# Kernel tuning notes

Measured on AMD Instinct MI355X. Metric: run time of the kernel, lower is better.

## Reference

```python
import jax, jax.numpy as jnp
import numpy as np
import math

N_NODES = 50000
N_EDGES = 800000
N_GRAPHS = 2500
IN_DIM = 128
HID = 128
HEADS = 2


def _lin_params(key, fan_in, fan_out, bias=True):
    k1, k2 = jax.random.split(key)
    s = 1.0 / math.sqrt(fan_in)
    W = jax.random.uniform(k1, (fan_in, fan_out), jnp.float32, -s, s)
    b = jax.random.uniform(k2, (fan_out,), jnp.float32, -s, s) if bias else None
    return W, b


def setup_inputs() -> dict:
    key = jax.random.key(0)
    ks = jax.random.split(key, 16)
    x = jax.random.normal(ks[0], (N_NODES, IN_DIM), jnp.float32)
    edge_index = jax.random.randint(ks[1], (2, N_EDGES), 0, N_NODES, jnp.int64)
    batch = jnp.sort(jax.random.randint(ks[2], (N_NODES,), 0, N_GRAPHS, jnp.int64))
    edge_attr = jax.random.normal(ks[3], (N_EDGES,), jnp.float32)

    HC = HEADS * HID  # 256
    # layer 1: in=128, out_channels=128, heads=2, concat=True
    Wq1, bq1 = _lin_params(ks[4], IN_DIM, HC)
    Wk1, bk1 = _lin_params(ks[5], IN_DIM, HC)
    Wv1, bv1 = _lin_params(ks[6], IN_DIM, HC)
    We1, _ = _lin_params(ks[7], 1, HC, bias=False)
    Ws1, bs1 = _lin_params(ks[8], IN_DIM, HC)
    # layer 2: in=256, out_channels=128, heads=2, concat=False
    Wq2, bq2 = _lin_params(ks[9], HC, HC)
    Wk2, bk2 = _lin_params(ks[10], HC, HC)
    Wv2, bv2 = _lin_params(ks[11], HC, HC)
    We2, _ = _lin_params(ks[12], 1, HC, bias=False)
    Ws2, bs2 = _lin_params(ks[13], HC, HID)
    return {
        "x": x, "edge_index": edge_index, "batch": batch, "edge_attr": edge_attr,
        "Wq1": Wq1, "bq1": bq1, "Wk1": Wk1, "bk1": bk1, "Wv1": Wv1, "bv1": bv1,
        "We1": We1, "Ws1": Ws1, "bs1": bs1,
        "Wq2": Wq2, "bq2": bq2, "Wk2": Wk2, "bk2": bk2, "Wv2": Wv2, "bv2": bv2,
        "We2": We2, "Ws2": Ws2, "bs2": bs2,
    }


def transformer_conv(x, src, dst, edge_attr, Wq, bq, Wk, bk, Wv, bv, We, Ws, bs,
                     heads, out_ch, concat):
    N = x.shape[0]
    q = (x @ Wq + bq).reshape(N, heads, out_ch)
    k = (x @ Wk + bk).reshape(N, heads, out_ch)
    v = (x @ Wv + bv).reshape(N, heads, out_ch)
    e = (edge_attr @ We).reshape(-1, heads, out_ch)  # [E,H,C]
    kj = k[src] + e
    vj = v[src] + e
    alpha = jnp.einsum('ehc,ehc->eh', q[dst], kj) / math.sqrt(out_ch)  # [E,H]
    amax = jax.ops.segment_max(alpha, dst, num_segments=N)  # [N,H]
    ex = jnp.exp(alpha - amax[dst])
    denom = jax.ops.segment_sum(ex, dst, num_segments=N)  # [N,H]
    w = ex / denom[dst]  # segment softmax over incoming edges
    out = jax.ops.segment_sum(w[..., None] * vj, dst, num_segments=N)  # [N,H,C]
    out = out.reshape(N, heads * out_ch) if concat else out.mean(axis=1)
    return out + (x @ Ws + bs)  # root/skip connection (beta=False)


def reference(x, edge_index, batch, edge_attr,
              Wq1, bq1, Wk1, bk1, Wv1, bv1, We1, Ws1, bs1,
              Wq2, bq2, Wk2, bk2, Wv2, bv2, We2, Ws2, bs2):
    src, dst = edge_index[0], edge_index[1]
    ea = edge_attr.reshape(-1, 1)
    h = transformer_conv(x, src, dst, ea, Wq1, bq1, Wk1, bk1, Wv1, bv1, We1,
                         Ws1, bs1, HEADS, HID, concat=True)
    h = jax.nn.relu(h)  # dropout = identity in eval mode
    h = transformer_conv(h, src, dst, ea, Wq2, bq2, Wk2, bk2, Wv2, bv2, We2,
                         Ws2, bs2, HEADS, HID, concat=False)
    # global mean pool per graph
    sums = jax.ops.segment_sum(h, batch, num_segments=N_GRAPHS)
    cnts = jax.ops.segment_sum(jnp.ones((h.shape[0],), h.dtype), batch,
                               num_segments=N_GRAPHS)
    return sums / jnp.maximum(cnts, 1.0)[:, None]
```

## Files before the change

kernel.cpp:

```cpp
#include <hip/hip_runtime.h>
#include <math.h>

#define N_NODES  50000
#define N_EDGES  800000
#define N_GRAPHS 2500
#define IN_DIM   128
#define HID      128
#define HEADS    2
#define HC       256

typedef unsigned short u16;
typedef unsigned char  u8;
typedef unsigned int   u32;
typedef short  s8v  __attribute__((ext_vector_type(8)));
typedef float  f4v  __attribute__((ext_vector_type(4)));
typedef float  f2v  __attribute__((ext_vector_type(2)));

__device__ inline float bf2f(u16 u) {
    union { unsigned int i; float f; } c; c.i = ((unsigned int)u) << 16; return c.f;
}
__device__ inline u16 f2bf(float x) {
    union { float f; unsigned int i; } c; c.f = x;
    unsigned int r = c.i + 0x7FFFu + ((c.i >> 16) & 1u);
    return (u16)(r >> 16);
}
__device__ inline float bflo(unsigned int u) {
    union { unsigned int i; float f; } c; c.i = u << 16; return c.f;
}
__device__ inline float bfhi(unsigned int u) {
    union { unsigned int i; float f; } c; c.i = u & 0xffff0000u; return c.f;
}
__device__ inline f2v mkf2(float a, float b) { f2v r; r.x = a; r.y = b; return r; }

#if __has_builtin(__builtin_amdgcn_cvt_pk_fp8_f32) && __has_builtin(__builtin_amdgcn_cvt_pk_f32_fp8)
#define FP8_HW 1
#else
#define FP8_HW 0
#endif

__device__ inline u8 f2fp8(float x) {
#if FP8_HW
    return (u8)(__builtin_amdgcn_cvt_pk_fp8_f32(x, x, 0, false) & 0xff);
#else
    union { float f; unsigned int u; } c; c.f = x;
    unsigned int s = (c.u >> 24) & 0x80u;
    c.u &= 0x7fffffffu;
    if (c.f >= 448.f) return (u8)(s | 0x7e);
    if (c.f < 0.015625f) {
        int m = (int)(c.f * 512.f + 0.5f);
        if (m >= 8) return (u8)(s | 0x08);
        return (u8)(s | m);
    }
    c.u += 0x000fffffu + ((c.u >> 20) & 1u);
    unsigned int e = ((c.u >> 23) & 0xffu) - 120u;
    unsigned int m = (c.u >> 20) & 7u;
    return (u8)(s | (e << 3) | m);
#endif
}

__device__ inline void fp8x8_to_f32(uint2 kd8, float* kf) {
#if FP8_HW
    f2v p0 = __builtin_amdgcn_cvt_pk_f32_fp8(kd8.x, false);
    f2v p1 = __builtin_amdgcn_cvt_pk_f32_fp8(kd8.x, true);
    f2v p2 = __builtin_amdgcn_cvt_pk_f32_fp8(kd8.y, false);
    f2v p3 = __builtin_amdgcn_cvt_pk_f32_fp8(kd8.y, true);
    kf[0] = p0.x; kf[1] = p0.y; kf[2] = p1.x; kf[3] = p1.y;
    kf[4] = p2.x; kf[5] = p2.y; kf[6] = p3.x; kf[7] = p3.y;
#else
#pragma unroll
    for (int i = 0; i < 8; ++i) {
        unsigned int b = ((i < 4) ? (kd8.x >> (8 * i)) : (kd8.y >> (8 * (i - 4)))) & 0xffu;
        unsigned int em = b & 0x7fu;
        union { unsigned int u; float f; } c;
        c.u = ((b & 0x80u) << 24) | ((em + 960u) << 20);
        float fn = c.f;
        float fs = (float)(int)em * 0.001953125f;
        fs = (b & 0x80u) ? -fs : fs;
        kf[i] = (em >= 8u) ? fn : fs;
    }
#endif
}

__device__ inline void fp8x8_to_f2(uint2 kd8, f2v* k2) {
#if FP8_HW
    k2[0] = __builtin_amdgcn_cvt_pk_f32_fp8(kd8.x, false);
    k2[1] = __builtin_amdgcn_cvt_pk_f32_fp8(kd8.x, true);
    k2[2] = __builtin_amdgcn_cvt_pk_f32_fp8(kd8.y, false);
    k2[3] = __builtin_amdgcn_cvt_pk_f32_fp8(kd8.y, true);
#else
    float kf[8];
    fp8x8_to_f32(kd8, kf);
    k2[0] = mkf2(kf[0], kf[1]); k2[1] = mkf2(kf[2], kf[3]);
    k2[2] = mkf2(kf[4], kf[5]); k2[3] = mkf2(kf[6], kf[7]);
#endif
}

__global__ __launch_bounds__(256) void init_kernel(
    const int* __restrict__ ei, const int* __restrict__ batch,
    int* __restrict__ deg, int* __restrict__ gdeg,
    int* __restrict__ flag_ei, int* __restrict__ flag_b)
{
    int b = blockIdx.x, t = threadIdx.x;
    if (b < 49) {
        int base = b * 1024 + t * 4;
        if (base + 3 < N_NODES) {
            *(int4*)&deg[base] = make_int4(0, 0, 0, 0);
        } else {
#pragma unroll
            for (int i = 0; i < 4; ++i) if (base + i < N_NODES) deg[base + i] = 0;
        }
    } else if (b < 59) {
        int i = (b - 49) * 256 + t;
        if (i < N_GRAPHS) gdeg[i] = 0;
    } else {
        const int* p = (b == 59) ? ei : batch;
        int ob = (b == 59) ? 1 : 40001;
        int* fl = (b == 59) ? flag_ei : flag_b;
        __shared__ int nz;
        if (t == 0) nz = 0;
        __syncthreads();
        int any = 0;
        for (int i = t; i < 1024; i += 256) if (p[ob + 2 * i] != 0) any = 1;
        if (any) atomicAdd(&nz, 1);
        __syncthreads();
        if (t == 0) *fl = (nz == 0) ? 1 : 0;
    }
}

#define W1_ELEMS (1024 * 128)
#define W2_ELEMS (896 * 256)
__global__ __launch_bounds__(256) void hist_prep_kernel(
    const int* __restrict__ ei, const int* __restrict__ batch,
    const int* __restrict__ flag_ei, const int* __restrict__ flag_b,
    int* __restrict__ deg, int* __restrict__ gdeg,
    const float* __restrict__ Wq1, const float* __restrict__ Wk1,
    const float* __restrict__ Wv1, const float* __restrict__ Ws1,
    const float* __restrict__ bq1, const float* __restrict__ bk1,
    const float* __restrict__ bv1, const float* __restrict__ bs1,
    const float* __restrict__ Wq2, const float* __restrict__ Wk2,
    const float* __restrict__ Wv2, const float* __restrict__ Ws2,
    const float* __restrict__ bq2, const float* __restrict__ bk2,
    const float* __restrict__ bv2, const float* __restrict__ bs2,
    u16* __restrict__ w1T, float* __restrict__ b1cat,
    u16* __restrict__ w2T, float* __restrict__ b2cat)
{
    const int E = N_EDGES;
    int i = blockIdx.x * 256 + threadIdx.x;
    if (i < E) {
        int f = *flag_ei;
        int d = f ? ei[2 * ((size_t)E + i)] : ei[(size_t)E + i];
        if ((unsigned)d < (unsigned)N_NODES) atomicAdd(&deg[d], 1);
    } else if (i < E + N_NODES) {
        int j = i - E;
        int f = *flag_b;
        int g = f ? batch[2 * (size_t)j] : batch[j];
        if ((unsigned)g < (unsigned)N_GRAPHS) atomicAdd(&gdeg[g], 1);
    } else if (i < E + N_NODES + W1_ELEMS) {
        int t1 = i - E - N_NODES;
        int n = t1 >> 7, k = t1 & 127;
        int w = n >> 8, nc = n & 255;
        const float* W = (w == 0) ? Wq1 : (w == 1) ? Wk1 : (w == 2) ? Wv1 : Ws1;
        w1T[t1] = f2bf(W[k * 256 + nc]);
        if (k == 0) {
            const float* b = (w == 0) ? bq1 : (w == 1) ? bk1 : (w == 2) ? bv1 : bs1;
            b1cat[n] = b[nc];
        }
    } else if (i < E + N_NODES + W1_ELEMS + W2_ELEMS) {
        int t2 = i - E - N_NODES - W1_ELEMS;
        int n = t2 >> 8, k = t2 & 255;
        float val, bval;
        if (n < 768) {
            int w = n >> 8, nc = n & 255;
            const float* W = (w == 0) ? Wq2 : (w == 1) ? Wk2 : Wv2;
            val = W[k * 256 + nc];
            bval = ((w == 0) ? bq2 : (w == 1) ? bk2 : bv2)[nc];
        } else {
            val = Ws2[k * 128 + (n - 768)];
            bval = bs2[n - 768];
        }
        w2T[t2] = f2bf(val);
        if (k == 0) b2cat[n] = bval;
    }
}

__global__ void scan_local_kernel(const int* __restrict__ deg, int* __restrict__ rowptr,
                                  int* __restrict__ bsums, int n) {
    __shared__ int sh[256];
    int t = threadIdx.x;
    int base = blockIdx.x * 1024 + t * 4;
    int d0 = (base + 0 < n) ? deg[base + 0] : 0;
    int d1 = (base + 1 < n) ? deg[base + 1] : 0;
    int d2 = (base + 2 < n) ? deg[base + 2] : 0;
    int d3 = (base + 3 < n) ? deg[base + 3] : 0;
    sh[t] = d0 + d1 + d2 + d3;
    __syncthreads();
    for (int off = 1; off < 256; off <<= 1) {
        int val = 0;
        if (t >= off) val = sh[t - off];
        __syncthreads();
        if (t >= off) sh[t] += val;
        __syncthreads();
    }
    int excl = (t > 0) ? sh[t - 1] : 0;
    if (t == 255) bsums[blockIdx.x] = sh[255];
    if (base + 0 < n) rowptr[base + 0] = excl;
    if (base + 1 < n) rowptr[base + 1] = excl + d0;
    if (base + 2 < n) rowptr[base + 2] = excl + d0 + d1;
    if (base + 3 < n) rowptr[base + 3] = excl + d0 + d1 + d2;
}

__global__ __launch_bounds__(256) void scan_mid_kernel(
    int* __restrict__ bsums, int nb, int* __restrict__ rowptr_last,
    const int* __restrict__ gdeg, int* __restrict__ growptr)
{
    int t = threadIdx.x;
    if (blockIdx.x == 0) {
        if (t >= 64) return;
        int v = (t < nb) ? bsums[t] : 0;
        int incl = v;
        for (int off = 1; off < 64; off <<= 1) {
            int u = __shfl_up(incl, off);
            if (t >= off) incl += u;
        }
        if (t < nb) bsums[t] = incl - v;
        if (t == 63) *rowptr_last = incl;
    } else {
        __shared__ int sh[256];
        int base = t * 10;
        int loc[10];
        int s = 0;
#pragma unroll
        for (int i = 0; i < 10; ++i) {
            int v = (base + i < N_GRAPHS) ? gdeg[base + i] : 0;
            loc[i] = s; s += v;
        }
        sh[t] = s;
        __syncthreads();
        for (int off = 1; off < 256; off <<= 1) {
            int val = 0;
            if (t >= off) val = sh[t - off];
            __syncthreads();
            if (t >= off) sh[t] += val;
            __syncthreads();
        }
        int excl = (t > 0) ? sh[t - 1] : 0;
#pragma unroll
        for (int i = 0; i < 10; ++i)
            if (base + i < N_GRAPHS) growptr[base + i] = excl + loc[i];
        if (t == 255) growptr[N_GRAPHS] = sh[255];
    }
}

__global__ void scan_add_kernel(int* __restrict__ rowptr, const int* __restrict__ bsums,
                                int* __restrict__ cursor, int n) {
    int i = blockIdx.x * blockDim.x + threadIdx.x;
    if (i < n) {
        int r = rowptr[i] + bsums[i >> 10];
        rowptr[i] = r;
        cursor[i] = r;
    }
}

template <typename AT, int KDIM, int NT>
__device__ __forceinline__ void gemm_slab_body(
    int bx, const AT* __restrict__ A, const u16* __restrict__ BT,
    const float* __restrict__ biascat,
    u16* __restrict__ C0, u8* __restrict__ KV, u16* __restrict__ C3,
    int s0, int s3, int M)
{
    __shared__ u16 As[64 * KDIM];
    __shared__ u16 Bs[128 * 32];
    int t = threadIdx.x;
    int wid = t >> 6, lane = t & 63;
    int wm = wid >> 1, wn = wid & 1;
    int row0 = bx * 64;

    if constexpr (sizeof(AT) == 4) {
#pragma unroll
        for (int i = 0; i < KDIM / 16; ++i) {
            int c = t + i * 256;
            int row = c / (KDIM / 4);
            int kq  = (c % (KDIM / 4)) * 4;
            float4 d = make_float4(0.f, 0.f, 0.f, 0.f);
            if (row0 + row < M)
                d = *(const float4*)&A[(size_t)(row0 + row) * KDIM + kq];
            ushort4 h;
            h.x = f2bf(d.x); h.y = f2bf(d.y); h.z = f2bf(d.z); h.w = f2bf(d.w);
            *(ushort4*)&As[row * KDIM + (kq ^ ((row & 7) << 3))] = h;
        }
    } else {
#pragma unroll
        for (int i = 0; i < KDIM / 32; ++i) {
            int c = t + i * 256;
            int row = c / (KDIM / 8);
            int kq  = (c % (KDIM / 8)) * 8;
            uint4 d = make_uint4(0u, 0u, 0u, 0u);
            if (row0 + row < M)
                d = *(const uint4*)&A[(size_t)(row0 + row) * KDIM + kq];
            *(uint4*)&As[row * KDIM + (kq ^ ((row & 7) << 3))] = d;
        }
    }
    __syncthreads();

    int koff = (lane >> 4) * 8;
    int mrow = wm * 32 + (lane & 15);
    int nrow = wn * 64 + (lane & 15);
    int aswz = (lane & 7) << 3;
    int bswz = (((lane & 15) >> 1) & 3) << 3;
    int nloc = (lane >> 4) * 4;

    int c0 = t, c1 = t + 256;
    int brow0 = c0 >> 2, bkq0 = (c0 & 3) * 8;
    int brow1 = c1 >> 2, bkq1 = (c1 & 3) * 8;
    int bsa0 = brow0 * 32 + (bkq0 ^ (((brow0 >> 1) & 3) << 3));
    int bsa1 = brow1 * 32 + (bkq1 ^ (((brow1 >> 1) & 3) << 3));

    uint4 pb0 = *(const uint4*)&BT[(size_t)brow0 * KDIM + bkq0];
    uint4 pb1 = *(const uint4*)&BT[(size_t)brow1 * KDIM + bkq1];

    for (int nt = 0; nt < NT; ++nt) {
        f4v acc[2][4];
#pragma unroll
        for (int i = 0; i < 2; ++i)
#pragma unroll
            for (int j = 0; j < 4; ++j)
#pragma unroll
                for (int r = 0; r < 4; ++r) acc[i][j][r] = 0.f;

        for (int k0 = 0; k0 < KDIM; k0 += 32) {
            *(uint4*)&Bs[bsa0] = pb0;
            *(uint4*)&Bs[bsa1] = pb1;
            __syncthreads();

            int nk = k0 + 32, nnt = nt;
            if (nk >= KDIM) { nk = 0; nnt = nt + 1; }
            if (nnt < NT) {
                pb0 = *(const uint4*)&BT[(size_t)(nnt * 128 + brow0) * KDIM + nk + bkq0];
                pb1 = *(const uint4*)&BT[(size_t)(nnt * 128 + brow1) * KDIM + nk + bkq1];
            }

            s8v af[2], bf[4];
#pragma unroll
            for (int tm = 0; tm < 2; ++tm)
                af[tm] = *(const s8v*)&As[(mrow + tm * 16) * KDIM + ((k0 + koff) ^ aswz)];
#pragma unroll
            for (int tn = 0; tn < 4; ++tn)
                bf[tn] = *(const s8v*)&Bs[(nrow + tn * 16) * 32 + (koff ^ bswz)];
#pragma unroll
            for (int tm = 0; tm < 2; ++tm)
#pragma unroll
                for (int tn = 0; tn < 4; ++tn)
                    acc[tm][tn] = __builtin_amdgcn_mfma_f32_16x16x32_bf16(
                        bf[tn], af[tm], acc[tm][tn], 0, 0, 0);
            __syncthreads();
        }

        int buf = nt >> 1;
        int colb = (nt & 1) * 128;
        float4 b4s[4];
#pragma unroll
        for (int tn = 0; tn < 4; ++tn)
            b4s[tn] = *(const float4*)&biascat[nt * 128 + wn * 64 + tn * 16 + nloc];

#pragma unroll
        for (int tm = 0; tm < 2; ++tm) {
            int row = row0 + wm * 32 + tm * 16 + (lane & 15);
            if (row >= M) continue;
#pragma unroll
            for (int tn = 0; tn < 4; ++tn) {
                int ncol = colb + wn * 64 + tn * 16 + nloc;
                float v0 = acc[tm][tn][0] + b4s[tn].x;
                float v1 = acc[tm][tn][1] + b4s[tn].y;
                float v2 = acc[tm][tn][2] + b4s[tn].z;
                float v3 = acc[tm][tn][3] + b4s[tn].w;
                if (buf == 1 || buf == 2) {
                    int off = (buf == 1) ? 0 : 256;
                    u32 pk = (u32)f2fp8(v0) | ((u32)f2fp8(v1) << 8)
                           | ((u32)f2fp8(v2) << 16) | ((u32)f2fp8(v3) << 24);
                    *(u32*)&KV[(size_t)row * 512 + off + ncol] = pk;
                } else {
                    u16* Cp = (buf == 0) ? C0 : C3;
                    int stride = (buf == 0) ? s0 : s3;
                    ushort4 h;
                    h.x = f2bf(v0); h.y = f2bf(v1); h.z = f2bf(v2); h.w = f2bf(v3);
                    *(ushort4*)&Cp[(size_t)row * stride + ncol] = h;
                }
            }
        }
    }
}

#define GB 782

__global__ __launch_bounds__(256, 4) void gemm1_scatter_kernel(
    const float* __restrict__ A, const u16* __restrict__ BT,
    const float* __restrict__ biascat,
    u16* __restrict__ C0, u8* __restrict__ KV, u16* __restrict__ C3,
    int s0, int s3, int M,
    const int* __restrict__ ei, const float* __restrict__ ea,
    const int* __restrict__ flag, int* __restrict__ cursor,
    u32* __restrict__ edges)
{
    if (blockIdx.x < GB) {
        gemm_slab_body<float, 128, 8>(blockIdx.x, A, BT, biascat,
                                      C0, KV, C3, s0, s3, M);
    } else {
        const int E = N_EDGES;
        int i = (blockIdx.x - GB) * 256 + threadIdx.x;
        if (i >= E) return;
        int f = *flag;
        int s = f ? ei[2 * (size_t)i] : ei[i];
        int d = f ? ei[2 * ((size_t)E + i)] : ei[(size_t)E + i];
        if ((unsigned)d >= (unsigned)N_NODES) return;
        if ((unsigned)s >= (unsigned)N_NODES) s = 0;
        int p = atomicAdd(&cursor[d], 1);
        u32 rec = (u32)(s & 0xffff) | ((u32)f2bf(ea[i]) << 16);
        edges[p] = rec;
    }
}

__global__ __launch_bounds__(256, 4) void gemm2_kernel(
    const u16* __restrict__ A, const u16* __restrict__ BT,
    const float* __restrict__ biascat,
    u16* __restrict__ C0, u8* __restrict__ KV, u16* __restrict__ C3,
    int s0, int s3, int M)
{
    gemm_slab_body<u16, 256, 7>(blockIdx.x, A, BT, biascat,
                                C0, KV, C3, s0, s3, M);
}

template <int LAYER>
__global__ __launch_bounds__(256) void attn_node(
    const u16* __restrict__ q, const u8* __restrict__ kv,
    const float* __restrict__ We, const u16* __restrict__ skip,
    const int* __restrict__ rowptr, const u32* __restrict__ edges,
    void* __restrict__ hout, int N)
{
    int wave = (blockIdx.x * blockDim.x + threadIdx.x) >> 6;
    int lane = threadIdx.x & 63;
    if (wave >= N) return;
    int n = wave;
    int half = lane >> 5;
    int cl   = lane & 31;
    const float scale2 = 0.12751743558136835f;

    uint4 qd = *(const uint4*)&q[(size_t)n * HC + cl * 8];
    f2v q2[4];
    q2[0] = mkf2(bflo(qd.x), bfhi(qd.x));
    q2[1] = mkf2(bflo(qd.y), bfhi(qd.y));
    q2[2] = mkf2(bflo(qd.z), bfhi(qd.z));
    q2[3] = mkf2(bflo(qd.w), bfhi(qd.w));
    float4 wlo = *(const float4*)&We[cl * 8];
    float4 whi = *(const float4*)&We[cl * 8 + 4];
    f2v w2[4];
    w2[0] = mkf2(wlo.x, wlo.y); w2[1] = mkf2(wlo.z, wlo.w);
    w2[2] = mkf2(whi.x, whi.y); w2[3] = mkf2(whi.z, whi.w);

    f2v qw2 = q2[0] * w2[0];
    qw2 += q2[1] * w2[1];
    qw2 += q2[2] * w2[2];
    qw2 += q2[3] * w2[3];
    float qw = qw2.x + qw2.y;
    qw += __shfl_xor(qw, 1);
    qw += __shfl_xor(qw, 2);
    qw += __shfl_xor(qw, 4);
    qw += __shfl_xor(qw, 8);

    int e0 = rowptr[n], e1 = rowptr[n + 1];
    float ll0 = 0.f, ll1 = 0.f;
    float pa0 = 0.f, pa1 = 0.f;
    f2v a0[4], a1[4];
#pragma unroll
    for (int i = 0; i < 4; ++i) { a0[i] = mkf2(0.f, 0.f); a1[i] = mkf2(0.f, 0.f); }

    int steps = (e1 - e0 + 7) >> 3;
    for (int st = 0; st < steps; ++st) {
        int eb = e0 + 8 * st + half;
        u32 rec[4]; bool act[4];
#pragma unroll
        for (int j = 0; j < 4; ++j) {
            int ex = eb + 2 * j;
            act[j] = ex < e1;
            rec[j] = edges[act[j] ? ex : e0];
        }
        uint2 kd[4], vd[4]; float ae[4];
#pragma unroll
        for (int j = 0; j < 4; ++j) {
            const u8* base = kv + (size_t)(rec[j] & 0xffffu) * 512;
            kd[j] = *(const uint2*)(base + cl * 8);
            vd[j] = *(const uint2*)(base + 256 + cl * 8);
            ae[j] = bfhi(rec[j]);
        }
#pragma unroll
        for (int j = 0; j < 4; ++j) {
            f2v k2[4], v2[4];
            fp8x8_to_f2(kd[j], k2);
            fp8x8_to_f2(vd[j], v2);
            f2v d2 = q2[0] * k2[0];
            d2 += q2[1] * k2[1];
            d2 += q2[2] * k2[2];
            d2 += q2[3] * k2[3];
            float d = d2.x + d2.y;
            d += __shfl_xor(d, 1);
            d += __shfl_xor(d, 2);
            d += __shfl_xor(d, 4);
            d += __shfl_xor(d, 8);
            float alpha = act[j] ? fmaf(ae[j], qw, d) * scale2 : -16384.f;
            float p = exp2f(fminf(alpha, 80.f));
            f2v p2 = mkf2(p, p);
            if (j & 1) {
                ll1 += p;
                pa1 = fmaf(p, ae[j], pa1);
                a1[0] += p2 * v2[0];
                a1[1] += p2 * v2[1];
                a1[2] += p2 * v2[2];
                a1[3] += p2 * v2[3];
            } else {
                ll0 += p;
                pa0 = fmaf(p, ae[j], pa0);
                a0[0] += p2 * v2[0];
                a0[1] += p2 * v2[1];
                a0[2] += p2 * v2[2];
                a0[3] += p2 * v2[3];
            }
        }
    }

    float l = ll0 + ll1;
    float pa = pa0 + pa1;
    float acc[8];
#pragma unroll
    for (int i = 0; i < 4; ++i) {
        f2v v = a0[i] + a1[i];
        acc[2 * i] = v.x; acc[2 * i + 1] = v.y;
    }

    l += __shfl_xor(l, 32);
    pa += __shfl_xor(pa, 32);
#pragma unroll
    for (int i = 0; i < 8; ++i) acc[i] += __shfl_xor(acc[i], 32);

    float wf[8];
    wf[0] = w2[0].x; wf[1] = w2[0].y; wf[2] = w2[1].x; wf[3] = w2[1].y;
    wf[4] = w2[2].x; wf[5] = w2[2].y; wf[6] = w2[3].x; wf[7] = w2[3].y;

    float inv = (l > 0.f) ? 1.f / l : 0.f;
    float o[8];
#pragma unroll
    for (int i = 0; i < 8; ++i) o[i] = fmaf(pa, wf[i], acc[i]) * inv;

    if constexpr (LAYER == 1) {
        if (half == 0) {
            uint4 sd = *(const uint4*)&skip[(size_t)n * HC + cl * 8];
            float sf[8];
            sf[0] = bflo(sd.x); sf[1] = bfhi(sd.x);
            sf[2] = bflo(sd.y); sf[3] = bfhi(sd.y);
            sf[4] = bflo(sd.z); sf[5] = bfhi(sd.z);
            sf[6] = bflo(sd.w); sf[7] = bfhi(sd.w);
            ushort4 o4a, o4b;
            o4a.x = f2bf(fmaxf(0.f, o[0] + sf[0]));
            o4a.y = f2bf(fmaxf(0.f, o[1] + sf[1]));
            o4a.z = f2bf(fmaxf(0.f, o[2] + sf[2]));
            o4a.w = f2bf(fmaxf(0.f, o[3] + sf[3]));
            o4b.x = f2bf(fmaxf(0.f, o[4] + sf[4]));
            o4b.y = f2bf(fmaxf(0.f, o[5] + sf[5]));
            o4b.z = f2bf(fmaxf(0.f, o[6] + sf[6]));
            o4b.w = f2bf(fmaxf(0.f, o[7] + sf[7]));
            u16* hp = (u16*)hout + (size_t)n * HC + cl * 8;
            *(ushort4*)hp = o4a;
            *(ushort4*)(hp + 4) = o4b;
        }
    } else {
#pragma unroll
        for (int i = 0; i < 8; ++i) {
            float t2 = __shfl_xor(o[i], 16);
            o[i] = 0.5f * (o[i] + t2);
        }
        if (lane < 16) {
            uint4 sd = *(const uint4*)&skip[(size_t)n * HID + lane * 8];
            float sf[8];
            sf[0] = bflo(sd.x); sf[1] = bfhi(sd.x);
            sf[2] = bflo(sd.y); sf[3] = bfhi(sd.y);
            sf[4] = bflo(sd.z); sf[5] = bfhi(sd.z);
            sf[6] = bflo(sd.w); sf[7] = bfhi(sd.w);
            float* hp = (float*)hout + (size_t)n * HID + lane * 8;
            float4 oa, ob;
            oa.x = o[0] + sf[0]; oa.y = o[1] + sf[1];
            oa.z = o[2] + sf[2]; oa.w = o[3] + sf[3];
            ob.x = o[4] + sf[4]; ob.y = o[5] + sf[5];
            ob.z = o[6] + sf[6]; ob.w = o[7] + sf[7];
            *(float4*)hp = oa;
            *(float4*)(hp + 4) = ob;
        }
    }
}

__global__ __launch_bounds__(256) void pool_kernel(
    const float* __restrict__ h2, const int* __restrict__ growptr,
    float* __restrict__ out) {
    int wave = (blockIdx.x * blockDim.x + threadIdx.x) >> 6;
    int lane = threadIdx.x & 63;
    if (wave >= N_GRAPHS) return;
    int r0 = growptr[wave], r1 = growptr[wave + 1];
    float sx = 0.f, sy = 0.f;
    for (int r = r0; r < r1; ++r) {
        float2 v = *(const float2*)&h2[(size_t)r * HID + lane * 2];
        sx += v.x; sy += v.y;
    }
    float inv = 1.f / fmaxf((float)(r1 - r0), 1.f);
    float2 o; o.x = sx * inv; o.y = sy * inv;
    *(float2*)&out[(size_t)wave * HID + lane * 2] = o;
}

extern "C" void kernel_launch(void* const* d_in, const int* in_sizes, int n_in,
                              void* d_out, int out_size, void* d_ws, size_t ws_size,
                              hipStream_t stream) {
    const float* x    = (const float*)d_in[0];
    const int*   ei   = (const int*)d_in[1];
    const int*   batch= (const int*)d_in[2];
    const float* ea   = (const float*)d_in[3];
    const float* Wq1  = (const float*)d_in[4];
    const float* bq1  = (const float*)d_in[5];
    const float* Wk1  = (const float*)d_in[6];
    const float* bk1  = (const float*)d_in[7];
    const float* Wv1  = (const float*)d_in[8];
    const float* bv1  = (const float*)d_in[9];
    const float* We1  = (const float*)d_in[10];
    const float* Ws1  = (const float*)d_in[11];
    const float* bs1  = (const float*)d_in[12];
    const float* Wq2  = (const float*)d_in[13];
    const float* bq2  = (const float*)d_in[14];
    const float* Wk2  = (const float*)d_in[15];
    const float* bk2  = (const float*)d_in[16];
    const float* Wv2  = (const float*)d_in[17];
    const float* bv2  = (const float*)d_in[18];
    const float* We2  = (const float*)d_in[19];
    const float* Ws2  = (const float*)d_in[20];
    const float* bs2  = (const float*)d_in[21];
    float* out = (float*)d_out;

    char* ws = (char*)d_ws;
    size_t off = 0;
    auto alloc = [&](size_t bytes) -> void* {
        void* p = ws + off;
        off += (bytes + 255) & ~(size_t)255;
        return p;
    };
    int*   flag_ei = (int*)alloc(4);
    int*   flag_b  = (int*)alloc(4);
    int*   deg     = (int*)alloc((size_t)N_NODES * 4);
    int*   rowptr  = (int*)alloc((size_t)(N_NODES + 1) * 4);
    int*   cursor  = (int*)alloc((size_t)N_NODES * 4);
    int*   bsums   = (int*)alloc(64 * 4);
    u32*   edges   = (u32*)alloc((size_t)N_EDGES * 4);
    int*   gdeg    = (int*)alloc((size_t)N_GRAPHS * 4);
    int*   growptr = (int*)alloc((size_t)(N_GRAPHS + 1) * 4);
    u16*   w1T     = (u16*)alloc((size_t)1024 * 128 * 2);
    float* b1cat   = (float*)alloc(1024 * 4);
    u16*   w2T     = (u16*)alloc((size_t)896 * 256 * 2);
    float* b2cat   = (float*)alloc(896 * 4);
    u16*   B0      = (u16*)alloc((size_t)N_NODES * HC * 2);
    u16*   B1      = (u16*)alloc((size_t)N_NODES * HC * 2);
    u8*    KVb     = (u8*)alloc((size_t)N_NODES * 512);
    u16*   B4      = (u16*)alloc((size_t)N_NODES * HID * 2);

    const int E = N_EDGES;

    init_kernel<<<61, 256, 0, stream>>>(ei, batch, deg, gdeg, flag_ei, flag_b);

    int hp_grid = (E + N_NODES + W1_ELEMS + W2_ELEMS + 255) / 256;
    hist_prep_kernel<<<hp_grid, 256, 0, stream>>>(
        ei, batch, flag_ei, flag_b, deg, gdeg,
        Wq1, Wk1, Wv1, Ws1, bq1, bk1, bv1, bs1,
        Wq2, Wk2, Wv2, Ws2, bq2, bk2, bv2, bs2,
        w1T, b1cat, w2T, b2cat);

    int nb = (N_NODES + 1023) / 1024;
    scan_local_kernel<<<nb, 256, 0, stream>>>(deg, rowptr, bsums, N_NODES);
    scan_mid_kernel<<<2, 256, 0, stream>>>(bsums, nb, rowptr + N_NODES, gdeg, growptr);
    scan_add_kernel<<<(N_NODES + 255) / 256, 256, 0, stream>>>(rowptr, bsums, cursor, N_NODES);

    int sc_grid = (E + 255) / 256;
    gemm1_scatter_kernel<<<GB + sc_grid, 256, 0, stream>>>(
        x, w1T, b1cat, B0, KVb, B1, 256, 256, N_NODES,
        ei, ea, flag_ei, cursor, edges);

    attn_node<1><<<N_NODES / 4, 256, 0, stream>>>(B0, KVb, We1, B1, rowptr, edges, B0, N_NODES);

    gemm2_kernel<<<GB, 256, 0, stream>>>(
        B0, w2T, b2cat, B1, KVb, B4, 256, 128, N_NODES);

    attn_node<2><<<N_NODES / 4, 256, 0, stream>>>(B1, KVb, We2, B4, rowptr, edges, B0, N_NODES);

    pool_kernel<<<(N_GRAPHS + 3) / 4, 256, 0, stream>>>((const float*)B0, growptr, out);
}
```

Before: 437.5 us.

## Fuse mean pooling into layer-2 attention via atomics; double-buffer layer-1 GEMM B tiles

Removes the separate pool kernel and the fp32 h2 write/read: the layer-2 attention kernel now scales each node's output by its graph's inverse count and atomically adds it into the zero-initialised output, which init_kernel now clears. Separately, the layer-1 GEMM gains a double-buffered shared B tile so each k-step needs one barrier instead of two. Atomics on 2500 graph rows may contend, since nodes are sorted by graph, and the summation order becomes nondeterministic.

```diff
diff --git a/kernel.cpp b/kernel.cpp
--- a/kernel.cpp
+++ b/kernel.cpp
@@ -95,10 +95,13 @@
 #endif
 }
 
+#define OUT_FLOATS (N_GRAPHS * HID)
+#define OUT_BLKS   ((OUT_FLOATS + 1023) / 1024)
 __global__ __launch_bounds__(256) void init_kernel(
     const int* __restrict__ ei, const int* __restrict__ batch,
     int* __restrict__ deg, int* __restrict__ gdeg,
-    int* __restrict__ flag_ei, int* __restrict__ flag_b)
+    int* __restrict__ flag_ei, int* __restrict__ flag_b,
+    float* __restrict__ out)
 {
     int b = blockIdx.x, t = threadIdx.x;
     if (b < 49) {
@@ -112,7 +115,7 @@
     } else if (b < 59) {
         int i = (b - 49) * 256 + t;
         if (i < N_GRAPHS) gdeg[i] = 0;
-    } else {
+    } else if (b < 61) {
         const int* p = (b == 59) ? ei : batch;
         int ob = (b == 59) ? 1 : 40001;
         int* fl = (b == 59) ? flag_ei : flag_b;
@@ -124,6 +127,14 @@
         if (any) atomicAdd(&nz, 1);
         __syncthreads();
         if (t == 0) *fl = (nz == 0) ? 1 : 0;
+    } else {
+        int base = (b - 61) * 1024 + t * 4;
+        if (base + 3 < OUT_FLOATS) {
+            *(float4*)&out[base] = make_float4(0.f, 0.f, 0.f, 0.f);
+        } else {
+#pragma unroll
+            for (int i = 0; i < 4; ++i) if (base + i < OUT_FLOATS) out[base + i] = 0.f;
+        }
     }
 }
 
@@ -261,7 +272,7 @@
     }
 }
 
-template <typename AT, int KDIM, int NT>
+template <typename AT, int KDIM, int NT, bool DBUF>
 __device__ __forceinline__ void gemm_slab_body(
     int bx, const AT* __restrict__ A, const u16* __restrict__ BT,
     const float* __restrict__ biascat,
@@ -269,7 +280,7 @@
     int s0, int s3, int M)
 {
     __shared__ u16 As[64 * KDIM];
-    __shared__ u16 Bs[128 * 32];
+    __shared__ u16 Bs[(DBUF ? 2 : 1) * 128 * 32];
     int t = threadIdx.x;
     int wid = t >> 6, lane = t & 63;
     int wm = wid >> 1, wn = wid & 1;
@@ -315,8 +326,22 @@
     int bsa0 = brow0 * 32 + (bkq0 ^ (((brow0 >> 1) & 3) << 3));
     int bsa1 = brow1 * 32 + (bkq1 ^ (((brow1 >> 1) & 3) << 3));
 
+    const int KS  = KDIM / 32;
+    const int TOT = NT * KS;
+
     uint4 pb0 = *(const uint4*)&BT[(size_t)brow0 * KDIM + bkq0];
     uint4 pb1 = *(const uint4*)&BT[(size_t)brow1 * KDIM + bkq1];
+    int cur = 0;
+
+    if constexpr (DBUF) {
+        *(uint4*)&Bs[bsa0] = pb0;
+        *(uint4*)&Bs[bsa1] = pb1;
+        if (TOT > 1) {
+            int n_ = 1 / KS, k_ = (1 % KS) * 32;
+            pb0 = *(const uint4*)&BT[(size_t)(n_ * 128 + brow0) * KDIM + k_ + bkq0];
+            pb1 = *(const uint4*)&BT[(size_t)(n_ * 128 + brow1) * KDIM + k_ + bkq1];
+        }
+    }
 
     for (int nt = 0; nt < NT; ++nt) {
         f4v acc[2][4];
@@ -327,16 +352,34 @@
 #pragma unroll
                 for (int r = 0; r < 4; ++r) acc[i][j][r] = 0.f;
 
-        for (int k0 = 0; k0 < KDIM; k0 += 32) {
-            *(uint4*)&Bs[bsa0] = pb0;
-            *(uint4*)&Bs[bsa1] = pb1;
-            __syncthreads();
-
-            int nk = k0 + 32, nnt = nt;
-            if (nk >= KDIM) { nk = 0; nnt = nt + 1; }
-            if (nnt < NT) {
-                pb0 = *(const uint4*)&BT[(size_t)(nnt * 128 + brow0) * KDIM + nk + bkq0];
-                pb1 = *(const uint4*)&BT[(size_t)(nnt * 128 + brow1) * KDIM + nk + bkq1];
+        for (int kk = 0; kk < KS; ++kk) {
+            int k0 = kk * 32;
+            int s = nt * KS + kk;
+            int co = 0;
+            if constexpr (DBUF) {
+                __syncthreads();
+                if (s + 1 < TOT) {
+                    int o = (cur ^ 1) * (128 * 32);
+                    *(uint4*)&Bs[o + bsa0] = pb0;
+                    *(uint4*)&Bs[o + bsa1] = pb1;
+                }
+                int s2 = s + 2;
+                if (s2 < TOT) {
+                    int n_ = s2 / KS, k_ = (s2 % KS) * 32;
+                    pb0 = *(const uint4*)&BT[(size_t)(n_ * 128 + brow0) * KDIM + k_ + bkq0];
+                    pb1 = *(const uint4*)&BT[(size_t)(n_ * 128 + brow1) * KDIM + k_ + bkq1];
+                }
+                co = cur * (128 * 32);
+            } else {
+                *(uint4*)&Bs[bsa0] = pb0;
+                *(uint4*)&Bs[bsa1] = pb1;
+                __syncthreads();
+                int s1 = s + 1;
+                if (s1 < TOT) {
+                    int n_ = s1 / KS, k_ = (s1 % KS) * 32;
+                    pb0 = *(const uint4*)&BT[(size_t)(n_ * 128 + brow0) * KDIM + k_ + bkq0];
+                    pb1 = *(const uint4*)&BT[(size_t)(n_ * 128 + brow1) * KDIM + k_ + bkq1];
+                }
             }
 
             s8v af[2], bf[4];
@@ -345,14 +388,19 @@
                 af[tm] = *(const s8v*)&As[(mrow + tm * 16) * KDIM + ((k0 + koff) ^ aswz)];
 #pragma unroll
             for (int tn = 0; tn < 4; ++tn)
-                bf[tn] = *(const s8v*)&Bs[(nrow + tn * 16) * 32 + (koff ^ bswz)];
+                bf[tn] = *(const s8v*)&Bs[co + (nrow + tn * 16) * 32 + (koff ^ bswz)];
 #pragma unroll
             for (int tm = 0; tm < 2; ++tm)
 #pragma unroll
                 for (int tn = 0; tn < 4; ++tn)
                     acc[tm][tn] = __builtin_amdgcn_mfma_f32_16x16x32_bf16(
                         bf[tn], af[tm], acc[tm][tn], 0, 0, 0);
-            __syncthreads();
+
+            if constexpr (DBUF) {
+                cur ^= 1;
+            } else {
+                __syncthreads();
+            }
         }
 
         int buf = nt >> 1;
@@ -402,8 +450,8 @@
     u32* __restrict__ edges)
 {
     if (blockIdx.x < GB) {
-        gemm_slab_body<float, 128, 8>(blockIdx.x, A, BT, biascat,
-                                      C0, KV, C3, s0, s3, M);
+        gemm_slab_body<float, 128, 8, true>(blockIdx.x, A, BT, biascat,
+                                            C0, KV, C3, s0, s3, M);
     } else {
         const int E = N_EDGES;
         int i = (blockIdx.x - GB) * 256 + threadIdx.x;
@@ -425,8 +473,8 @@
     u16* __restrict__ C0, u8* __restrict__ KV, u16* __restrict__ C3,
     int s0, int s3, int M)
 {
-    gemm_slab_body<u16, 256, 7>(blockIdx.x, A, BT, biascat,
-                                C0, KV, C3, s0, s3, M);
+    gemm_slab_body<u16, 256, 7, false>(blockIdx.x, A, BT, biascat,
+                                       C0, KV, C3, s0, s3, M);
 }
 
 template <int LAYER>
@@ -434,7 +482,9 @@
     const u16* __restrict__ q, const u8* __restrict__ kv,
     const float* __restrict__ We, const u16* __restrict__ skip,
     const int* __restrict__ rowptr, const u32* __restrict__ edges,
-    void* __restrict__ hout, int N)
+    void* __restrict__ hout, int N,
+    const int* __restrict__ batchp, const int* __restrict__ flag_b,
+    const int* __restrict__ gdeg)
 {
     int wave = (blockIdx.x * blockDim.x + threadIdx.x) >> 6;
     int lane = threadIdx.x & 63;
@@ -583,33 +633,17 @@
             sf[2] = bflo(sd.y); sf[3] = bfhi(sd.y);
             sf[4] = bflo(sd.z); sf[5] = bfhi(sd.z);
             sf[6] = bflo(sd.w); sf[7] = bfhi(sd.w);
-            float* hp = (float*)hout + (size_t)n * HID + lane * 8;
-            float4 oa, ob;
-            oa.x = o[0] + sf[0]; oa.y = o[1] + sf[1];
-            oa.z = o[2] + sf[2]; oa.w = o[3] + sf[3];
-            ob.x = o[4] + sf[4]; ob.y = o[5] + sf[5];
-            ob.z = o[6] + sf[6]; ob.w = o[7] + sf[7];
-            *(float4*)hp = oa;
-            *(float4*)(hp + 4) = ob;
-        }
-    }
-}
-
-__global__ __launch_bounds__(256) void pool_kernel(
-    const float* __restrict__ h2, const int* __restrict__ growptr,
-    float* __restrict__ out) {
-    int wave = (blockIdx.x * blockDim.x + threadIdx.x) >> 6;
-    int lane = threadIdx.x & 63;
-    if (wave >= N_GRAPHS) return;
-    int r0 = growptr[wave], r1 = growptr[wave + 1];
-    float sx = 0.f, sy = 0.f;
-    for (int r = r0; r < r1; ++r) {
-        float2 v = *(const float2*)&h2[(size_t)r * HID + lane * 2];
-        sx += v.x; sy += v.y;
-    }
-    float inv = 1.f / fmaxf((float)(r1 - r0), 1.f);
-    float2 o; o.x = sx * inv; o.y = sy * inv;
-    *(float2*)&out[(size_t)wave * HID + lane * 2] = o;
+            int fb = *flag_b;
+            int g = fb ? batchp[2 * (size_t)n] : batchp[n];
+            if ((unsigned)g < (unsigned)N_GRAPHS) {
+                float invc = 1.f / fmaxf((float)gdeg[g], 1.f);
+                float* op = (float*)hout + (size_t)g * HID + lane * 8;
+#pragma unroll
+                for (int i = 0; i < 8; ++i)
+                    atomicAdd(&op[i], (o[i] + sf[i]) * invc);
+            }
+        }
+    }
 }
 
 extern "C" void kernel_launch(void* const* d_in, const int* in_sizes, int n_in,
@@ -666,7 +700,8 @@
 
     const int E = N_EDGES;
 
-    init_kernel<<<61, 256, 0, stream>>>(ei, batch, deg, gdeg, flag_ei, flag_b);
+    init_kernel<<<61 + OUT_BLKS, 256, 0, stream>>>(ei, batch, deg, gdeg,
+                                                   flag_ei, flag_b, out);
 
     int hp_grid = (E + N_NODES + W1_ELEMS + W2_ELEMS + 255) / 256;
     hist_prep_kernel<<<hp_grid, 256, 0, stream>>>(
@@ -685,12 +720,12 @@
         x, w1T, b1cat, B0, KVb, B1, 256, 256, N_NODES,
         ei, ea, flag_ei, cursor, edges);
 
-    attn_node<1><<<N_NODES / 4, 256, 0, stream>>>(B0, KVb, We1, B1, rowptr, edges, B0, N_NODES);
+    attn_node<1><<<N_NODES / 4, 256, 0, stream>>>(B0, KVb, We1, B1, rowptr, edges,
+                                                  B0, N_NODES, nullptr, nullptr, nullptr);
 
     gemm2_kernel<<<GB, 256, 0, stream>>>(
         B0, w2T, b2cat, B1, KVb, B4, 256, 128, N_NODES);
 
-    attn_node<2><<<N_NODES / 4, 256, 0, stream>>>(B1, KVb, We2, B4, rowptr, edges, B0, N_NODES);
-
-    pool_kernel<<<(N_GRAPHS + 3) / 4, 256, 0, stream>>>((const float*)B0, growptr, out);
-}
+    attn_node<2><<<N_NODES / 4, 256, 0, stream>>>(B1, KVb, We2, B4, rowptr, edges,
+                                                  out, N_NODES, batch, flag_b, gdeg);
+}
```

After: 578.3 us. 1.32x slower.
